# Kernel optimization log

Measured on AMD Instinct MI355X. Metric: run time of the kernel, lower is better.

## Reference

```python
import jax, jax.numpy as jnp
import numpy as np

N_SAMPLES = 16384
L = 8000   # num pseudo labels
C = 8      # num cameras
D = 256    # feature dim
N = 512    # batch size
T = 0.05   # temperature
K = 50     # hard_neg_k
LW = 0.5   # inter-cam loss weight


def setup_inputs() -> dict:
    key = jax.random.key(0)
    k1, k2, k3, k4, k5 = jax.random.split(key, 5)
    feats = jax.random.normal(k1, (N, D), dtype=jnp.float32)
    indexes = jax.random.randint(k2, (N,), 0, N_SAMPLES)
    label_table = jax.random.randint(k3, (N_SAMPLES,), 0, L)
    cam_table = jax.random.randint(k4, (N_SAMPLES,), 0, C)
    centers = jax.random.normal(k5, (L * C, D), dtype=jnp.float32)
    centers = centers / jnp.linalg.norm(centers, axis=1, keepdims=True)
    return {"feats": feats, "indexes": indexes, "label_table": label_table,
            "cam_table": cam_table, "centers": centers}


def reference(feats, indexes, label_table, cam_table, centers):
    # F.normalize(feats, p=2, dim=1)
    feats = feats / jnp.linalg.norm(feats, axis=1, keepdims=True)
    labels = label_table[indexes]          # [n]
    cams = cam_table[indexes]              # [n]
    cen = jax.lax.stop_gradient(centers)   # centers are a non-grad buffer in torch

    all_sims = feats @ cen.T               # [n, P]  P = L*C, proxy(l,c) = l*C + c
    n, P = all_sims.shape
    sims_r = all_sims.reshape(n, L, C)     # [n, L, C]

    # ---- intra-camera loss: softmax over the L proxies sharing sample's camera ----
    idx_cam = jnp.broadcast_to(cams[:, None, None], (n, L, 1))
    sims_intra = jnp.take_along_axis(sims_r, idx_cam, axis=2)[..., 0]  # [n, L]
    logp_intra = jax.nn.log_softmax(sims_intra / T, axis=1)
    loss_intra_i = -jnp.take_along_axis(logp_intra, labels[:, None], axis=1)[:, 0]

    # ---- inter-camera loss: C positives (same label, all cams) + top-K hard negatives ----
    idx_lab = jnp.broadcast_to(labels[:, None, None], (n, 1, C))
    pos_sims = jnp.take_along_axis(sims_r, idx_lab, axis=1)[:, 0, :]   # [n, C]
    masked = jnp.where(jnp.arange(L)[None, :, None] == labels[:, None, None],
                       jnp.float32(-10000.0), sims_r).reshape(n, P)
    neg_sims, _ = jax.lax.top_k(masked, K)                             # [n, K]
    logits = jnp.concatenate([pos_sims, neg_sims], axis=1) / T         # [n, C+K]
    logp = jax.nn.log_softmax(logits, axis=1)
    loss_inter_i = -jnp.mean(logp[:, :C], axis=1)  # target = 1/C on the C positives

    # ---- per-camera mean, summed over cameras (matches the torch.unique loop) ----
    ones = jnp.ones((n,), feats.dtype)
    counts = jax.ops.segment_sum(ones, cams, num_segments=C)
    safe = jnp.maximum(counts, 1.0)
    s_intra = jax.ops.segment_sum(loss_intra_i, cams, num_segments=C)
    s_inter = jax.ops.segment_sum(loss_inter_i, cams, num_segments=C)
    loss_intra = jnp.sum(jnp.where(counts > 0, s_intra / safe, 0.0))
    loss_inter = LW * jnp.sum(jnp.where(counts > 0, s_inter / safe, 0.0))
    return jnp.stack([loss_intra, loss_inter])
```

## Files before the change

kernel.cpp:

```cpp
#include <hip/hip_runtime.h>
#include <stdint.h>

#define NS   512
#define DDIM 256
#define LL   8000
#define CC   8
#define PP   64000
#define KTOP 50
#define CAP  1024
#define BM   128
#define BN   128
#define NCT  (PP/BN)
#define K2C  28.853900817779268f

typedef float f32x4 __attribute__((ext_vector_type(4)));
typedef short bf16x8 __attribute__((ext_vector_type(8)));

__device__ __forceinline__ ushort f2bf(float x) {
    uint32_t b = __float_as_uint(x);
    b += 0x7fffu + ((b >> 16) & 1u);
    return (ushort)(b >> 16);
}
__device__ __forceinline__ float bf2f(ushort u) {
    return __uint_as_float(((uint32_t)u) << 16);
}

__global__ void k_norm_gather(const float* __restrict__ feats,
                              const int* __restrict__ indexes,
                              const int* __restrict__ ltab,
                              const int* __restrict__ ctab,
                              ushort* __restrict__ feats_b,
                              int* __restrict__ labels,
                              int* __restrict__ cams,
                              int* __restrict__ gcount) {
    const int n = blockIdx.x;
    const int lane = threadIdx.x;
    f32x4 v = ((const f32x4*)(feats + (size_t)n * DDIM))[lane];
    float ss = v[0]*v[0] + v[1]*v[1] + v[2]*v[2] + v[3]*v[3];
#pragma unroll
    for (int off = 32; off > 0; off >>= 1) ss += __shfl_down(ss, off);
    float tot = __shfl(ss, 0);
    float sc = 1.0f / sqrtf(tot);
    ushort4 o;
    o.x = f2bf(v[0] * sc); o.y = f2bf(v[1] * sc);
    o.z = f2bf(v[2] * sc); o.w = f2bf(v[3] * sc);
    ((ushort4*)(feats_b + (size_t)n * DDIM))[lane] = o;
    if (lane == 0) {
        int idx = indexes[n];
        labels[n] = ltab[idx];
        cams[n] = ctab[idx];
        gcount[n] = 0;
    }
}

__global__ __launch_bounds__(256, 2)
void k_gemm_fused(const ushort* __restrict__ A, const float* __restrict__ B,
                  const int* __restrict__ labels, const int* __restrict__ cams,
                  float* __restrict__ partial, float* __restrict__ cand,
                  int* __restrict__ gcount, float* __restrict__ posbuf) {
    const int ct = blockIdx.x;
    const int rt = blockIdx.y;
    const int C0 = ct * BN;
    const int R0 = rt * BM;
    const int tid  = threadIdx.x;
    const int lane = tid & 63;
    const int w    = tid >> 6;
    const int wm   = w >> 1;
    const int wn   = w & 1;
    const int lr   = lane & 15;
    const int lk   = lane >> 4;

    __shared__ ushort sA[BM][264];
    __shared__ ushort sB[BN][36];
    __shared__ int    s_lab[BM];
    __shared__ int    s_cam[BM];
    __shared__ float  s_intra[BM];
    __shared__ float  s_wred[8];
    __shared__ float  s_tau;

#pragma unroll
    for (int it = 0; it < 16; ++it) {
        int q   = tid + it * 256;
        int row = q >> 5;
        int c16 = q & 31;
        *(bf16x8*)(&sA[row][c16 * 8]) =
            *(const bf16x8*)(A + (size_t)(R0 + row) * DDIM + c16 * 8);
    }
    if (tid < BM) {
        s_lab[tid] = labels[R0 + tid];
        s_cam[tid] = cams[R0 + tid];
        s_intra[tid] = 0.0f;
    }

#pragma unroll
    for (int it = 0; it < 4; ++it) {
        int q   = tid + it * 256;
        int col = q >> 3;
        int k4  = q & 7;
        f32x4 v = *(const f32x4*)(B + (size_t)(C0 + col) * DDIM + k4 * 4);
        ushort4 o = { f2bf(v[0]), f2bf(v[1]), f2bf(v[2]), f2bf(v[3]) };
        *(ushort4*)(&sB[col][k4 * 4]) = o;
    }
    __syncthreads();

    f32x4 zero = {0.f, 0.f, 0.f, 0.f};
    f32x4 acc[4][4];
#pragma unroll
    for (int m = 0; m < 4; ++m)
#pragma unroll
        for (int nn = 0; nn < 4; ++nn) acc[m][nn] = zero;

    for (int ks = 0; ks < 8; ++ks) {
        bf16x8 af[4], bf[4];
#pragma unroll
        for (int m = 0; m < 4; ++m)
            af[m] = *(const bf16x8*)(&sA[wm * 64 + m * 16 + lr][ks * 32 + lk * 8]);
#pragma unroll
        for (int nn = 0; nn < 4; ++nn)
            bf[nn] = *(const bf16x8*)(&sB[wn * 64 + nn * 16 + lr][lk * 8]);
#pragma unroll
        for (int m = 0; m < 4; ++m)
#pragma unroll
            for (int nn = 0; nn < 4; ++nn)
                acc[m][nn] = __builtin_amdgcn_mfma_f32_16x16x32_bf16(af[m], bf[nn], acc[m][nn], 0, 0, 0);
        if (ks < 7) {
            __syncthreads();
#pragma unroll
            for (int it = 0; it < 4; ++it) {
                int q   = tid + it * 256;
                int col = q >> 3;
                int k4  = q & 7;
                f32x4 v = *(const f32x4*)(B + (size_t)(C0 + col) * DDIM + (ks + 1) * 32 + k4 * 4);
                ushort4 o = { f2bf(v[0]), f2bf(v[1]), f2bf(v[2]), f2bf(v[3]) };
                *(ushort4*)(&sB[col][k4 * 4]) = o;
            }
            __syncthreads();
        }
    }

    float ss = 0.0f, sc2 = 0.0f;
#pragma unroll
    for (int m = 0; m < 4; ++m)
#pragma unroll
        for (int nn = 0; nn < 4; ++nn)
#pragma unroll
            for (int j = 0; j < 4; ++j) {
                float v = acc[m][nn][j];
                if (fabsf(v) < 0.25f) { ss += v * v; sc2 += 1.0f; }
            }
#pragma unroll
    for (int off = 32; off > 0; off >>= 1) {
        ss  += __shfl_down(ss, off);
        sc2 += __shfl_down(sc2, off);
    }
    if (lane == 0) { s_wred[w] = ss; s_wred[4 + w] = sc2; }
    __syncthreads();
    if (tid == 0) {
        float S = s_wred[0] + s_wred[1] + s_wred[2] + s_wred[3];
        float C = s_wred[4] + s_wred[5] + s_wred[6] + s_wred[7];
        s_tau = 2.9f * sqrtf(S / fmaxf(C, 1.0f));
    }
    __syncthreads();
    const float tau = s_tau;

#pragma unroll
    for (int m = 0; m < 4; ++m) {
#pragma unroll
        for (int j = 0; j < 4; ++j) {
            const int rl  = wm * 64 + m * 16 + lk * 4 + j;
            const int r   = R0 + rl;
            const int lab = s_lab[rl];
            const int cm  = s_cam[rl];
            const bool mycam = ((lr & 7) == cm);
            float isum = 0.0f;
#pragma unroll
            for (int nn = 0; nn < 4; ++nn) {
                const int c_loc = wn * 64 + nn * 16 + lr;
                const float v = acc[m][nn][j];
                if (mycam) isum += exp2f(v * K2C);
                const int g = (C0 + c_loc) >> 3;
                if (g == lab) {
                    posbuf[r * CC + (c_loc & 7)] = v;
                } else if (v > tau) {
                    int id = atomicAdd(&gcount[r], 1);
                    if (id < CAP) cand[(size_t)r * CAP + id] = v;
                }
            }
            if (mycam) atomicAdd(&s_intra[rl], isum);
        }
    }
    __syncthreads();
    if (tid < BM) partial[(size_t)ct * NS + R0 + tid] = s_intra[tid];
}

__global__ __launch_bounds__(256)
void k_row(const ushort* __restrict__ fb, const float* __restrict__ B,
           const float* __restrict__ partial, const float* __restrict__ cand,
           const int* __restrict__ gcount, const float* __restrict__ posbuf,
           const int* __restrict__ labels, const int* __restrict__ cams,
           float* __restrict__ li, float* __restrict__ le) {
    const int n = blockIdx.x;
    const int tid = threadIdx.x;
    __shared__ float red[256];
    __shared__ int   redi[256];
    __shared__ float spos[CC];
    __shared__ float scand[CAP];
    __shared__ float f[DDIM];
    __shared__ float s_lo, s_hi;
    __shared__ int   s_done, s_cnt;

    float s = 0.0f;
    for (int b = tid; b < NCT; b += 256) s += partial[(size_t)b * NS + n];
    red[tid] = s;
    __syncthreads();
    for (int off = 128; off > 0; off >>= 1) {
        if (tid < off) red[tid] += red[tid + off];
        __syncthreads();
    }
    if (tid < CC) spos[tid] = posbuf[n * CC + tid];
    __syncthreads();
    if (tid == 0) li[n] = logf(red[0]) - 20.0f * spos[cams[n]];

    int c = gcount[n];
    if (c >= KTOP && c <= CAP) {
        for (int i = tid; i < c; i += 256) scand[i] = cand[(size_t)n * CAP + i];
    } else {
        if (tid < DDIM) f[tid] = bf2f(fb[(size_t)n * DDIM + tid]);
        const int label = labels[n];
        if (tid == 0) { s_lo = -1.01f; s_hi = 1.01f; s_done = 0; s_cnt = 0; }
        __syncthreads();
        for (int it = 0; it < 16; ++it) {
            if (s_done) break;
            float tm = 0.5f * (s_lo + s_hi);
            int cnt = 0;
            for (int p = tid; p < PP; p += 256) {
                if ((p >> 3) == label) continue;
                const float* col = B + (size_t)p * DDIM;
                float d = 0.0f;
                for (int k = 0; k < DDIM; ++k) d += f[k] * bf2f(f2bf(col[k]));
                cnt += (d > tm);
            }
            redi[tid] = cnt;
            __syncthreads();
            for (int off = 128; off > 0; off >>= 1) {
                if (tid < off) redi[tid] += redi[tid + off];
                __syncthreads();
            }
            int tot = redi[0];
            __syncthreads();
            if (tot >= KTOP && tot <= CAP) {
                if (tid == 0) s_cnt = 0;
                __syncthreads();
                for (int p = tid; p < PP; p += 256) {
                    if ((p >> 3) == label) continue;
                    const float* col = B + (size_t)p * DDIM;
                    float d = 0.0f;
                    for (int k = 0; k < DDIM; ++k) d += f[k] * bf2f(f2bf(col[k]));
                    if (d > tm) {
                        int id = atomicAdd(&s_cnt, 1);
                        if (id < CAP) scand[id] = d;
                    }
                }
                __syncthreads();
                if (tid == 0) s_done = 1;
            } else {
                if (tid == 0) { if (tot < KTOP) s_hi = tm; else s_lo = tm; }
            }
            __syncthreads();
        }
        if (!s_done) {
            if (tid == 0) s_cnt = 0;
            __syncthreads();
            float tl = s_lo;
            for (int p = tid; p < PP; p += 256) {
                if ((p >> 3) == label) continue;
                const float* col = B + (size_t)p * DDIM;
                float d = 0.0f;
                for (int k = 0; k < DDIM; ++k) d += f[k] * bf2f(f2bf(col[k]));
                if (d > tl) {
                    int id = atomicAdd(&s_cnt, 1);
                    if (id < CAP) scand[id] = d;
                }
            }
        }
        __syncthreads();
        c = s_cnt;
        if (c > CAP) c = CAP;
    }
    __syncthreads();

    float sum = 0.0f;
    for (int i = tid; i < c; i += 256) {
        float v = scand[i];
        int rk = 0;
        for (int j = 0; j < c; ++j) {
            float u = scand[j];
            rk += (u > v) || (u == v && j < i);
        }
        if (rk < KTOP) sum += exp2f(v * K2C);
    }
    if (tid < CC) sum += exp2f(spos[tid] * K2C);
    red[tid] = sum;
    __syncthreads();
    for (int off = 128; off > 0; off >>= 1) {
        if (tid < off) red[tid] += red[tid + off];
        __syncthreads();
    }
    if (tid == 0) {
        float ps = 0.0f;
#pragma unroll
        for (int j = 0; j < CC; ++j) ps += spos[j];
        le[n] = logf(red[0]) - 2.5f * ps;
    }
}

__global__ void k_finalize(const float* __restrict__ li, const float* __restrict__ le,
                           const int* __restrict__ cams, float* __restrict__ out) {
    __shared__ float si[CC], se[CC];
    __shared__ int sc[CC];
    int tid = threadIdx.x;
    if (tid < CC) { si[tid] = 0.f; se[tid] = 0.f; sc[tid] = 0; }
    __syncthreads();
    for (int i = tid; i < NS; i += 256) {
        int cm = cams[i];
        atomicAdd(&si[cm], li[i]);
        atomicAdd(&se[cm], le[i]);
        atomicAdd(&sc[cm], 1);
    }
    __syncthreads();
    if (tid == 0) {
        float a = 0.f, b = 0.f;
        for (int cm = 0; cm < CC; ++cm) {
            if (sc[cm] > 0) {
                a += si[cm] / (float)sc[cm];
                b += se[cm] / (float)sc[cm];
            }
        }
        out[0] = a;
        out[1] = 0.5f * b;
    }
}

extern "C" void kernel_launch(void* const* d_in, const int* in_sizes, int n_in,
                              void* d_out, int out_size, void* d_ws, size_t ws_size,
                              hipStream_t stream) {
    const float* feats   = (const float*)d_in[0];
    const int*   indexes = (const int*)d_in[1];
    const int*   ltab    = (const int*)d_in[2];
    const int*   ctab    = (const int*)d_in[3];
    const float* centers = (const float*)d_in[4];
    float* out = (float*)d_out;

    char* p = (char*)d_ws;
    float*  cand    = (float*)p;   p += (size_t)NS * CAP * sizeof(float);
    float*  partial = (float*)p;   p += (size_t)NCT * NS * sizeof(float);
    float*  posbuf  = (float*)p;   p += (size_t)NS * CC * sizeof(float);
    ushort* fb      = (ushort*)p;  p += (size_t)NS * DDIM * sizeof(ushort);
    int*    labels  = (int*)p;     p += 2048;
    int*    cams    = (int*)p;     p += 2048;
    float*  li      = (float*)p;   p += 2048;
    float*  le      = (float*)p;   p += 2048;
    int*    gcount  = (int*)p;     p += 2048;

    hipLaunchKernelGGL(k_norm_gather, dim3(NS), dim3(64), 0, stream,
                       feats, indexes, ltab, ctab, fb, labels, cams, gcount);
    hipLaunchKernelGGL(k_gemm_fused, dim3(NCT, 4), dim3(256), 0, stream,
                       fb, centers, labels, cams, partial, cand, gcount, posbuf);
    hipLaunchKernelGGL(k_row, dim3(NS), dim3(256), 0, stream,
                       fb, centers, partial, cand, gcount, posbuf, labels, cams, li, le);
    hipLaunchKernelGGL(k_finalize, dim3(1), dim3(256), 0, stream, li, le, cams, out);
}
```

Measured before the change: 238.1 us.

## Pre-convert centers to bf16 and load GEMM fragments directly from global memory

Adds a separate kernel that converts the whole fp32 centers matrix to bf16 once per call into workspace. The fused GEMM then drops its shared-memory staging and barriers and loads A and B MFMA fragments straight from global memory. Each wave now owns a 128x32 output strip instead of a 64x64 quadrant. This removes the repeated per-block fp32-to-bf16 conversion (each centers tile was converted four times, once per row tile) and the synchronisation. In exchange it adds an extra pass writing and reading a 32 MB bf16 buffer, and the fragment loads from global memory are uncoalesced with less on-chip reuse.

```diff
diff --git a/kernel.cpp b/kernel.cpp
--- a/kernel.cpp
+++ b/kernel.cpp
@@ -8,13 +8,12 @@
 #define PP   64000
 #define KTOP 50
 #define CAP  1024
-#define BM   128
-#define BN   128
-#define NCT  (PP/BN)
+#define NCT  500
 #define K2C  28.853900817779268f
 
 typedef float f32x4 __attribute__((ext_vector_type(4)));
 typedef short bf16x8 __attribute__((ext_vector_type(8)));
+typedef short short8 __attribute__((ext_vector_type(8)));
 
 __device__ __forceinline__ ushort f2bf(float x) {
     uint32_t b = __float_as_uint(x);
@@ -53,96 +52,74 @@
     }
 }
 
-__global__ __launch_bounds__(256, 2)
-void k_gemm_fused(const ushort* __restrict__ A, const float* __restrict__ B,
-                  const int* __restrict__ labels, const int* __restrict__ cams,
-                  float* __restrict__ partial, float* __restrict__ cand,
-                  int* __restrict__ gcount, float* __restrict__ posbuf) {
-    const int ct = blockIdx.x;
-    const int rt = blockIdx.y;
-    const int C0 = ct * BN;
-    const int R0 = rt * BM;
-    const int tid  = threadIdx.x;
-    const int lane = tid & 63;
-    const int w    = tid >> 6;
-    const int wm   = w >> 1;
-    const int wn   = w & 1;
+__global__ __launch_bounds__(256) void k_conv(const float* __restrict__ c,
+                                              ushort* __restrict__ cb) {
+    const size_t NCHUNK = (size_t)PP * DDIM / 8;
+    size_t i = (size_t)blockIdx.x * blockDim.x + threadIdx.x;
+    const size_t step = (size_t)gridDim.x * blockDim.x;
+    for (; i < NCHUNK; i += step) {
+        size_t base = i * 8;
+        f32x4 a = *(const f32x4*)(c + base);
+        f32x4 b = *(const f32x4*)(c + base + 4);
+        short8 r;
+        r[0] = (short)f2bf(a[0]); r[1] = (short)f2bf(a[1]);
+        r[2] = (short)f2bf(a[2]); r[3] = (short)f2bf(a[3]);
+        r[4] = (short)f2bf(b[0]); r[5] = (short)f2bf(b[1]);
+        r[6] = (short)f2bf(b[2]); r[7] = (short)f2bf(b[3]);
+        *(short8*)(cb + base) = r;
+    }
+}
+
+__global__ void k_gemm_fused(const ushort* __restrict__ A, const ushort* __restrict__ B,
+                             const int* __restrict__ labels, const int* __restrict__ cams,
+                             float* __restrict__ partial, float* __restrict__ cand,
+                             int* __restrict__ gcount, float* __restrict__ posbuf) {
+    const int lane = threadIdx.x & 63;
+    const int w    = threadIdx.x >> 6;
     const int lr   = lane & 15;
     const int lk   = lane >> 4;
-
-    __shared__ ushort sA[BM][264];
-    __shared__ ushort sB[BN][36];
-    __shared__ int    s_lab[BM];
-    __shared__ int    s_cam[BM];
-    __shared__ float  s_intra[BM];
-    __shared__ float  s_wred[8];
-    __shared__ float  s_tau;
-
-#pragma unroll
-    for (int it = 0; it < 16; ++it) {
-        int q   = tid + it * 256;
-        int row = q >> 5;
-        int c16 = q & 31;
-        *(bf16x8*)(&sA[row][c16 * 8]) =
-            *(const bf16x8*)(A + (size_t)(R0 + row) * DDIM + c16 * 8);
-    }
-    if (tid < BM) {
-        s_lab[tid] = labels[R0 + tid];
-        s_cam[tid] = cams[R0 + tid];
+    const int bRow = blockIdx.y * 128;
+    const int C0   = blockIdx.x * 128;
+    const int cBase = C0 + w * 32;
+    const int tid  = threadIdx.x;
+
+    __shared__ int   s_lab[128];
+    __shared__ int   s_cam[128];
+    __shared__ float s_intra[128];
+    __shared__ float s_wred[8];
+    __shared__ float s_tau;
+
+    if (tid < 128) {
+        s_lab[tid] = labels[bRow + tid];
+        s_cam[tid] = cams[bRow + tid];
         s_intra[tid] = 0.0f;
     }
 
-#pragma unroll
-    for (int it = 0; it < 4; ++it) {
-        int q   = tid + it * 256;
-        int col = q >> 3;
-        int k4  = q & 7;
-        f32x4 v = *(const f32x4*)(B + (size_t)(C0 + col) * DDIM + k4 * 4);
-        ushort4 o = { f2bf(v[0]), f2bf(v[1]), f2bf(v[2]), f2bf(v[3]) };
-        *(ushort4*)(&sB[col][k4 * 4]) = o;
-    }
-    __syncthreads();
-
     f32x4 zero = {0.f, 0.f, 0.f, 0.f};
-    f32x4 acc[4][4];
-#pragma unroll
-    for (int m = 0; m < 4; ++m)
-#pragma unroll
-        for (int nn = 0; nn < 4; ++nn) acc[m][nn] = zero;
-
-    for (int ks = 0; ks < 8; ++ks) {
-        bf16x8 af[4], bf[4];
-#pragma unroll
-        for (int m = 0; m < 4; ++m)
-            af[m] = *(const bf16x8*)(&sA[wm * 64 + m * 16 + lr][ks * 32 + lk * 8]);
-#pragma unroll
-        for (int nn = 0; nn < 4; ++nn)
-            bf[nn] = *(const bf16x8*)(&sB[wn * 64 + nn * 16 + lr][lk * 8]);
-#pragma unroll
-        for (int m = 0; m < 4; ++m)
-#pragma unroll
-            for (int nn = 0; nn < 4; ++nn)
-                acc[m][nn] = __builtin_amdgcn_mfma_f32_16x16x32_bf16(af[m], bf[nn], acc[m][nn], 0, 0, 0);
-        if (ks < 7) {
-            __syncthreads();
-#pragma unroll
-            for (int it = 0; it < 4; ++it) {
-                int q   = tid + it * 256;
-                int col = q >> 3;
-                int k4  = q & 7;
-                f32x4 v = *(const f32x4*)(B + (size_t)(C0 + col) * DDIM + (ks + 1) * 32 + k4 * 4);
-                ushort4 o = { f2bf(v[0]), f2bf(v[1]), f2bf(v[2]), f2bf(v[3]) };
-                *(ushort4*)(&sB[col][k4 * 4]) = o;
-            }
-            __syncthreads();
+    f32x4 acc[8][2];
+#pragma unroll
+    for (int m = 0; m < 8; ++m) { acc[m][0] = zero; acc[m][1] = zero; }
+
+#pragma unroll
+    for (int kb = 0; kb < 8; ++kb) {
+        const int kpos = kb * 32 + lk * 8;
+        bf16x8 bfr[2];
+#pragma unroll
+        for (int nn = 0; nn < 2; ++nn)
+            bfr[nn] = *(const bf16x8*)(B + (size_t)(cBase + nn * 16 + lr) * DDIM + kpos);
+#pragma unroll
+        for (int m = 0; m < 8; ++m) {
+            bf16x8 afr = *(const bf16x8*)(A + (size_t)(bRow + m * 16 + lr) * DDIM + kpos);
+            acc[m][0] = __builtin_amdgcn_mfma_f32_16x16x32_bf16(afr, bfr[0], acc[m][0], 0, 0, 0);
+            acc[m][1] = __builtin_amdgcn_mfma_f32_16x16x32_bf16(afr, bfr[1], acc[m][1], 0, 0, 0);
         }
     }
 
     float ss = 0.0f, sc2 = 0.0f;
 #pragma unroll
-    for (int m = 0; m < 4; ++m)
-#pragma unroll
-        for (int nn = 0; nn < 4; ++nn)
+    for (int m = 0; m < 8; ++m)
+#pragma unroll
+        for (int nn = 0; nn < 2; ++nn)
 #pragma unroll
             for (int j = 0; j < 4; ++j) {
                 float v = acc[m][nn][j];
@@ -164,18 +141,18 @@
     const float tau = s_tau;
 
 #pragma unroll
-    for (int m = 0; m < 4; ++m) {
+    for (int m = 0; m < 8; ++m) {
 #pragma unroll
         for (int j = 0; j < 4; ++j) {
-            const int rl  = wm * 64 + m * 16 + lk * 4 + j;
-            const int r   = R0 + rl;
+            const int rl  = m * 16 + lk * 4 + j;
+            const int r   = bRow + rl;
             const int lab = s_lab[rl];
             const int cm  = s_cam[rl];
             const bool mycam = ((lr & 7) == cm);
             float isum = 0.0f;
 #pragma unroll
-            for (int nn = 0; nn < 4; ++nn) {
-                const int c_loc = wn * 64 + nn * 16 + lr;
+            for (int nn = 0; nn < 2; ++nn) {
+                const int c_loc = w * 32 + nn * 16 + lr;
                 const float v = acc[m][nn][j];
                 if (mycam) isum += exp2f(v * K2C);
                 const int g = (C0 + c_loc) >> 3;
@@ -190,7 +167,7 @@
         }
     }
     __syncthreads();
-    if (tid < BM) partial[(size_t)ct * NS + R0 + tid] = s_intra[tid];
+    if (tid < 128) partial[(size_t)blockIdx.x * NS + bRow + tid] = s_intra[tid];
 }
 
 __global__ __launch_bounds__(256)
@@ -352,6 +329,7 @@
     float* out = (float*)d_out;
 
     char* p = (char*)d_ws;
+    ushort* cb      = (ushort*)p;  p += (size_t)PP * DDIM * sizeof(ushort);
     float*  cand    = (float*)p;   p += (size_t)NS * CAP * sizeof(float);
     float*  partial = (float*)p;   p += (size_t)NCT * NS * sizeof(float);
     float*  posbuf  = (float*)p;   p += (size_t)NS * CC * sizeof(float);
@@ -364,8 +342,9 @@
 
     hipLaunchKernelGGL(k_norm_gather, dim3(NS), dim3(64), 0, stream,
                        feats, indexes, ltab, ctab, fb, labels, cams, gcount);
+    hipLaunchKernelGGL(k_conv, dim3(2048), dim3(256), 0, stream, centers, cb);
     hipLaunchKernelGGL(k_gemm_fused, dim3(NCT, 4), dim3(256), 0, stream,
-                       fb, centers, labels, cams, partial, cand, gcount, posbuf);
+                       fb, cb, labels, cams, partial, cand, gcount, posbuf);
     hipLaunchKernelGGL(k_row, dim3(NS), dim3(256), 0, stream,
                        fb, centers, partial, cand, gcount, posbuf, labels, cams, li, le);
     hipLaunchKernelGGL(k_finalize, dim3(1), dim3(256), 0, stream, li, le, cams, out);
```

Result: slower. 289.8 us (+21.7%).
